# Optimization experiments

Measured on AMD Instinct MI355X. Metric: run time of the kernel, lower is better.

The kernel has to match this reference:

```python
import jax, jax.numpy as jnp
import numpy as np

EMBED_DIM = 2048
HEAD_DIM = 128
B, T = 4, 2048


def setup_inputs() -> dict:
    key = jax.random.key(0)
    k1, k2, k3, k4 = jax.random.split(key, 4)
    x_in = jax.random.normal(k1, (B, T, EMBED_DIM), dtype=jnp.float32)
    scale = 1.0 / np.sqrt(EMBED_DIM)
    Wq = jax.random.normal(k2, (EMBED_DIM, HEAD_DIM), dtype=jnp.float32) * scale
    Wk = jax.random.normal(k3, (EMBED_DIM, HEAD_DIM), dtype=jnp.float32) * scale
    Wv = jax.random.normal(k4, (EMBED_DIM, HEAD_DIM), dtype=jnp.float32) * scale
    return {"x_in": x_in, "Wq": Wq, "Wk": Wk, "Wv": Wv}


def reference(x_in, Wq, Wk, Wv):
    # x_in: [B, T, E]; projections (Linear, no bias)
    q = jnp.einsum('bte,ed->btd', x_in, Wq)  # [B,T,D]
    k = jnp.einsum('bte,ed->btd', x_in, Wk)
    v = jnp.einsum('bte,ed->btd', x_in, Wv)
    t = x_in.shape[1]
    d = Wq.shape[1]
    s = jnp.einsum('btd,bsd->bts', q, k) / jnp.sqrt(jnp.asarray(d, q.dtype))  # [B,Tq,Tk]
    # causal mask: positions with tril==0 (k index > q index) -> -inf
    causal = jnp.tril(jnp.ones((t, t), dtype=bool))
    s = jnp.where(causal, s, -jnp.inf)
    # NOTE: original module applies softmax over dim=1 (query axis), faithfully reproduced
    a = jax.nn.softmax(s, axis=1)
    z = jnp.einsum('bts,bsd->btd', a, v)  # [B,T,D]
    return z
```

## Files before the change

kernel.cpp:

```cpp
#include <hip/hip_runtime.h>

typedef _Float16 f16x8 __attribute__((ext_vector_type(8)));
typedef _Float16 f16x4 __attribute__((ext_vector_type(4)));
typedef float f32x4 __attribute__((ext_vector_type(4)));

#define T_DIM 2048
#define E_DIM 2048
#define D_DIM 128
#define NB 4
#define KSP_P 4
#define KCH_P 512
#define KSP_A 8
#define KCH_A 256
#define NCH2 32

__device__ __forceinline__ void gll16(const void* g, void* l) {
  __builtin_amdgcn_global_load_lds(
      (const __attribute__((address_space(1))) unsigned int*)g,
      (__attribute__((address_space(3))) unsigned int*)l, 16, 0, 0);
}

__device__ __forceinline__ void merge_stat(float& m, float& l, float pm, float pl) {
  if (pm != -__builtin_inff()) {
    float nm = fmaxf(m, pm);
    l = l * __expf(m - nm) + pl * __expf(pm - nm);
    m = nm;
  }
}


__global__ void prep(const float* __restrict__ Wq, const float* __restrict__ Wk,
                     const float* __restrict__ Wv, _Float16* __restrict__ WhT,
                     float* __restrict__ Z) {
  int idx = blockIdx.x * 256 + threadIdx.x;
  int y = blockIdx.y;
  if (y < 3) {
    const float* W = (y == 0) ? Wq : ((y == 1) ? Wk : Wv);
    int e = idx & (E_DIM - 1), d = idx >> 11;
    WhT[(size_t)y * (D_DIM * E_DIM) + idx] = (_Float16)W[e * D_DIM + d];
  } else {
    f32x4 z = {0.f, 0.f, 0.f, 0.f};
    *(f32x4*)(Z + (size_t)idx * 4) = z;
  }
}


__global__ __launch_bounds__(384) void proj_gemm(
    const float* __restrict__ x, const _Float16* __restrict__ WhT,
    _Float16* __restrict__ Ph) {
  __shared__ _Float16 A16[2][64 * 32];
  __shared__ _Float16 Bsw[2][384 * 32];
  const int tid = threadIdx.x, w = tid >> 6, lane = tid & 63;
  const int wn = w, quad = lane >> 4, l16 = lane & 15;
  const int t0 = blockIdx.x * 64;
  const int ks = blockIdx.y;
  const int kb = ks * KCH_P;
  const int arow = tid >> 2, aseg = tid & 3;
  const int asw = (aseg ^ ((arow >> 1) & 3)) * 8;
  const int br = tid >> 2, bseg = tid & 3;

  f32x4 ax0, ax1;
  auto loadA = [&](int k0) {
    if (tid < 256) {
      const float* src = x + (size_t)(t0 + arow) * E_DIM + k0 + aseg * 8;
      ax0 = *(const f32x4*)src;
      ax1 = *(const f32x4*)(src + 4);
    }
  };
  auto writeA = [&](int buf) {
    if (tid < 256) {
      f16x8 o;
#pragma unroll
      for (int e = 0; e < 4; ++e) {
        o[e] = (_Float16)ax0[e];
        o[e + 4] = (_Float16)ax1[e];
      }
      *(f16x8*)(&A16[buf][arow * 32 + asw]) = o;
    }
  };
  auto stageB = [&](int buf, int k0) {
#pragma unroll
    for (int p = 0; p < 4; ++p) {
      int r = p * 96 + br;
      int g = bseg ^ ((r >> 1) & 3);
      gll16(WhT + (size_t)r * E_DIM + k0 + g * 8, &Bsw[buf][r * 32 + bseg * 8]);
    }
  };

  f32x4 acc[4][4] = {};
  loadA(kb);
  stageB(0, kb);
  asm volatile("s_waitcnt vmcnt(0)" ::: "memory");
  writeA(0);
  const int NIT = KCH_P / 32;
  for (int it = 0; it < NIT; ++it) {
    const int cur = it & 1;
    __syncthreads();
    if (it + 1 < NIT) {
      loadA(kb + (it + 1) * 32);
      stageB(cur ^ 1, kb + (it + 1) * 32);
    }
    f16x8 af[4], bf[4];
#pragma unroll
    for (int i = 0; i < 4; ++i) {
      int row = i * 16 + l16;
      int sg = (quad ^ ((row >> 1) & 3)) * 8;
      af[i] = *(const f16x8*)(&A16[cur][row * 32 + sg]);
    }
#pragma unroll
    for (int j = 0; j < 4; ++j) {
      int row = wn * 64 + j * 16 + l16;
      int sg = (quad ^ ((row >> 1) & 3)) * 8;
      bf[j] = *(const f16x8*)(&Bsw[cur][row * 32 + sg]);
    }
    __builtin_amdgcn_s_setprio(1);
#pragma unroll
    for (int i = 0; i < 4; ++i)
#pragma unroll
      for (int j = 0; j < 4; ++j)
        acc[i][j] = __builtin_amdgcn_mfma_f32_16x16x32_f16(af[i], bf[j], acc[i][j], 0, 0, 0);
    __builtin_amdgcn_s_setprio(0);
    if (it + 1 < NIT) {
      asm volatile("s_waitcnt vmcnt(0)" ::: "memory");
      writeA(cur ^ 1);
    }
  }
  const int mat = wn >> 1;
  const int nb0 = (wn & 1) * 64;
  _Float16* P = Ph + ((size_t)(ks * 3 + mat) << 20);
  if (mat < 2) {
#pragma unroll
    for (int i = 0; i < 4; ++i)
#pragma unroll
      for (int j = 0; j < 4; ++j) {
        int n = nb0 + j * 16 + l16;
#pragma unroll
        for (int r = 0; r < 4; ++r) {
          int t = t0 + i * 16 + quad * 4 + r;
          P[(size_t)t * D_DIM + n] = (_Float16)acc[i][j][r];
        }
      }
  } else {
#pragma unroll
    for (int i = 0; i < 4; ++i)
#pragma unroll
      for (int j = 0; j < 4; ++j) {
        int n = nb0 + j * 16 + l16;
        int t = t0 + i * 16 + quad * 4;
        f16x4 o;
#pragma unroll
        for (int r = 0; r < 4; ++r) o[r] = (_Float16)acc[i][j][r];
        *(f16x4*)(P + ((size_t)(t >> 11) * D_DIM + n) * T_DIM + (t & (T_DIM - 1))) = o;
      }
  }
}


__global__ void proj_reduce(const _Float16* __restrict__ Ph, _Float16* __restrict__ Qh,
                            _Float16* __restrict__ Kh, _Float16* __restrict__ VT) {
  size_t u = ((size_t)blockIdx.x * 256 + threadIdx.x) * 8;
  int mat = (int)(u >> 20);
  size_t rem = u & ((1u << 20) - 1);
  float s[8] = {};
#pragma unroll
  for (int ks = 0; ks < KSP_P; ++ks) {
    f16x8 p = *(const f16x8*)(Ph + ((size_t)(ks * 3 + mat) << 20) + rem);
#pragma unroll
    for (int e = 0; e < 8; ++e) s[e] += (float)p[e];
  }
  f16x8 o;
#pragma unroll
  for (int e = 0; e < 8; ++e) o[e] = (_Float16)s[e];
  _Float16* dst = (mat == 0) ? Qh : ((mat == 1) ? Kh : VT);
  *(f16x8*)(dst + rem) = o;
}


__global__ __launch_bounds__(256) void s_gemm(const _Float16* __restrict__ Qh,
                                              const _Float16* __restrict__ Kh,
                                              _Float16* __restrict__ S,
                                              float* __restrict__ Pm,
                                              float* __restrict__ Pl) {
  int idx = blockIdx.x;
  int xt = (int)((sqrtf(8.f * idx + 1.f) - 1.f) * 0.5f);
  while ((xt + 1) * (xt + 2) / 2 <= idx) ++xt;
  while (xt * (xt + 1) / 2 > idx) --xt;
  int yt = idx - xt * (xt + 1) / 2;
  __shared__ _Float16 Bs[4][128 * 32];
  const int tid = threadIdx.x, w = tid >> 6, lane = tid & 63;
  const int wr = w >> 1, wc = w & 1, quad = lane >> 4, l16 = lane & 15;
  const int t0 = xt * 128, s0 = yt * 128, b = blockIdx.y;
  const _Float16* A = Qh + (size_t)b * T_DIM * D_DIM;
  const _Float16* B = Kh + (size_t)b * T_DIM * D_DIM;
  const int srow = lane >> 2;
  const int swz = ((lane & 3) ^ ((srow >> 1) & 3)) * 8;
#pragma unroll
  for (int kq = 0; kq < 4; ++kq)
#pragma unroll
    for (int q = 0; q < 2; ++q) {
      int rbase = w * 32 + q * 16;
      gll16(B + (size_t)(s0 + rbase + srow) * D_DIM + kq * 32 + swz,
            Bs[kq] + rbase * 32);
    }
  __syncthreads();
  f32x4 acc[4][4] = {};
  const int bsg = (quad ^ ((l16 >> 1) & 3)) * 8;
#pragma unroll
  for (int kq = 0; kq < 4; ++kq) {
    f16x8 af[4], bf[4];
#pragma unroll
    for (int i = 0; i < 4; ++i)
      af[i] = *(const f16x8*)(A + (size_t)(t0 + wr * 64 + i * 16 + l16) * D_DIM +
                              kq * 32 + quad * 8);
#pragma unroll
    for (int j = 0; j < 4; ++j)
      bf[j] = *(const f16x8*)(Bs[kq] + (wc * 64 + j * 16 + l16) * 32 + bsg);
#pragma unroll
    for (int i = 0; i < 4; ++i)
#pragma unroll
      for (int j = 0; j < 4; ++j)
        acc[i][j] = __builtin_amdgcn_mfma_f32_16x16x32_f16(af[i], bf[j], acc[i][j], 0, 0, 0);
  }
  _Float16* Sb = S + (size_t)b * T_DIM * T_DIM;
  const float scale = 0.08838834764831845f;
  const float NEG = -__builtin_inff();
#pragma unroll
  for (int j = 0; j < 4; ++j) {
    const int s = s0 + wc * 64 + j * 16 + l16;
    float vv[16];
    float m = NEG;
#pragma unroll
    for (int i = 0; i < 4; ++i)
#pragma unroll
      for (int r = 0; r < 4; ++r) {
        int t = t0 + wr * 64 + i * 16 + quad * 4 + r;
        float v = (s > t) ? NEG : acc[i][j][r] * scale;
        Sb[(size_t)t * T_DIM + s] = (_Float16)v;
        vv[i * 4 + r] = v;
        m = fmaxf(m, v);
      }
    float l = 0.f;
    if (m != NEG) {
#pragma unroll
      for (int k = 0; k < 16; ++k) l += __expf(vv[k] - m);
    }
#pragma unroll
    for (int d = 16; d <= 32; d <<= 1) {
      float pm = __shfl_xor(m, d, 64);
      float pl = __shfl_xor(l, d, 64);
      merge_stat(m, l, pm, pl);
    }
    if (quad == 0) {
      int c = 2 * xt + wr;
      Pm[((size_t)c * NB + b) * T_DIM + s] = m;
      Pl[((size_t)c * NB + b) * T_DIM + s] = l;
    }
  }
}


__global__ __launch_bounds__(256) void av_gemm(const _Float16* __restrict__ S,
                                               const _Float16* __restrict__ VT,
                                               const float* __restrict__ Pm,
                                               const float* __restrict__ Pl,
                                               float* __restrict__ Z) {
  const int t0 = blockIdx.x * 128, b = blockIdx.y, ks = blockIdx.z;
  const int Kmax = t0 + 128;
  const int Kstart = ks * KCH_A;
  if (Kstart >= Kmax) return;
  const int Kend = (Kstart + KCH_A < Kmax) ? (Kstart + KCH_A) : Kmax;
  const int nit = (Kend - Kstart) >> 5;
  __shared__ _Float16 As[2][128 * 32];
  __shared__ _Float16 Bs[2][128 * 32];
  __shared__ float Ms[KCH_A];
  __shared__ float Ls[KCH_A];
  const int tid = threadIdx.x, w = tid >> 6, lane = tid & 63;
  const int wr = w >> 1, wc = w & 1, quad = lane >> 4, l16 = lane & 15;
  const _Float16* Sb = S + (size_t)b * T_DIM * T_DIM;
  const _Float16* Vb = VT + (size_t)b * D_DIM * T_DIM;
  {
    const int s = Kstart + tid;
    const int c0 = s >> 6;
    float m = -__builtin_inff(), l = 0.f;
    for (int base = c0 & ~7; base < NCH2; base += 8) {
      float pm[8], pl[8];
#pragma unroll
      for (int k = 0; k < 8; ++k) {
        size_t pidx = ((size_t)(base + k) * NB + b) * T_DIM + s;
        pm[k] = Pm[pidx];
        pl[k] = Pl[pidx];
      }
#pragma unroll
      for (int k = 0; k < 8; ++k)
        if (base + k >= c0) merge_stat(m, l, pm[k], pl[k]);
    }
    Ms[tid] = m;
    Ls[tid] = 1.f / l;
  }
  __syncthreads();
  const int srow = lane >> 2;
  const int arow = tid >> 2, aseg = tid & 3;
  const int asw = (aseg ^ ((arow >> 1) & 3)) * 8;
  f16x8 sv0, sv1;
  auto loadS = [&](int k0) {
    sv0 = *(const f16x8*)(Sb + (size_t)(t0 + arow) * T_DIM + k0 + aseg * 8);
    sv1 = *(const f16x8*)(Sb + (size_t)(t0 + 64 + arow) * T_DIM + k0 + aseg * 8);
  };
  auto stageB = [&](int buf, int k0) {
#pragma unroll
    for (int q = 0; q < 2; ++q) {
      int rbase = w * 32 + q * 16;
      int row = rbase + srow;
      int g = ((lane & 3) ^ ((row >> 1) & 3)) * 8;
      gll16(Vb + (size_t)row * T_DIM + k0 + g, Bs[buf] + rbase * 32);
    }
  };
  auto writeA = [&](int buf, int k0) {
#pragma unroll
    for (int q = 0; q < 2; ++q) {
      f16x8 v = q ? sv1 : sv0;
      f16x8 o;
#pragma unroll
      for (int e = 0; e < 8; ++e) {
        int li = k0 + aseg * 8 + e - Kstart;
        o[e] = (_Float16)(__expf((float)v[e] - Ms[li]) * Ls[li]);
      }
      *(f16x8*)(As[buf] + (q * 64 + arow) * 32 + asw) = o;
    }
  };
  f32x4 acc[4][4] = {};
  loadS(Kstart);
  stageB(0, Kstart);
  asm volatile("s_waitcnt vmcnt(0)" ::: "memory");
  writeA(0, Kstart);
  for (int it = 0; it < nit; ++it) {
    const int cur = it & 1;
    const int k0 = Kstart + it * 32;
    __syncthreads();
    if (it + 1 < nit) {
      loadS(k0 + 32);
      stageB(cur ^ 1, k0 + 32);
    }
    f16x8 af[4], bf[4];
#pragma unroll
    for (int i = 0; i < 4; ++i) {
      int row = wr * 64 + i * 16 + l16;
      int sg = (quad ^ ((row >> 1) & 3)) * 8;
      af[i] = *(const f16x8*)(As[cur] + row * 32 + sg);
    }
#pragma unroll
    for (int j = 0; j < 4; ++j) {
      int row = wc * 64 + j * 16 + l16;
      int sg = (quad ^ ((row >> 1) & 3)) * 8;
      bf[j] = *(const f16x8*)(Bs[cur] + row * 32 + sg);
    }
    __builtin_amdgcn_s_setprio(1);
#pragma unroll
    for (int i = 0; i < 4; ++i)
#pragma unroll
      for (int j = 0; j < 4; ++j)
        acc[i][j] = __builtin_amdgcn_mfma_f32_16x16x32_f16(af[i], bf[j], acc[i][j], 0, 0, 0);
    __builtin_amdgcn_s_setprio(0);
    if (it + 1 < nit) {
      asm volatile("s_waitcnt vmcnt(0)" ::: "memory");
      writeA(cur ^ 1, k0 + 32);
    }
  }
  float* Zb = Z + (size_t)b * T_DIM * D_DIM;
#pragma unroll
  for (int i = 0; i < 4; ++i)
#pragma unroll
    for (int j = 0; j < 4; ++j) {
      int n = wc * 64 + j * 16 + l16;
#pragma unroll
      for (int r = 0; r < 4; ++r) {
        int t = t0 + wr * 64 + i * 16 + quad * 4 + r;
        atomicAdd(&Zb[(size_t)t * D_DIM + n], acc[i][j][r]);
      }
    }
}


extern "C" void kernel_launch(void* const* d_in, const int* in_sizes, int n_in,
                              void* d_out, int out_size, void* d_ws, size_t ws_size,
                              hipStream_t stream) {
  const float* x = (const float*)d_in[0];
  const float* Wq = (const float*)d_in[1];
  const float* Wk = (const float*)d_in[2];
  const float* Wv = (const float*)d_in[3];
  char* ws = (char*)d_ws;
  _Float16* WhT = (_Float16*)(ws + 33554432);
  _Float16* Qh = (_Float16*)(ws + 35127296);
  _Float16* Kh = (_Float16*)(ws + 37224448);
  _Float16* VT = (_Float16*)(ws + 39321600);
  _Float16* S = (_Float16*)(ws + 41418752);
  _Float16* Ph = (_Float16*)(ws + 41418752);
  float* Pm = (float*)(ws + 75038720);
  float* Pl = (float*)(ws + 76087296);
  float* Z = (float*)d_out;

  prep<<<dim3(1024, 4), 256, 0, stream>>>(Wq, Wk, Wv, WhT, Z);
  proj_gemm<<<dim3(128, KSP_P), 384, 0, stream>>>(x, WhT, Ph);
  proj_reduce<<<1536, 256, 0, stream>>>(Ph, Qh, Kh, VT);
  s_gemm<<<dim3(136, 4), 256, 0, stream>>>(Qh, Kh, S, Pm, Pl);
  av_gemm<<<dim3(16, 4, KSP_A), 256, 0, stream>>>(S, VT, Pm, Pl, Z);
}
```

Baseline: 185.2 us.

## Stage fp32 x via direct-to-LDS loads, single-buffer proj GEMM, double K split

After: 336.8 us. 81.9% more time.

```diff
diff --git a/kernel.cpp b/kernel.cpp
--- a/kernel.cpp
+++ b/kernel.cpp
@@ -8,8 +8,8 @@
 #define E_DIM 2048
 #define D_DIM 128
 #define NB 4
-#define KSP_P 4
-#define KCH_P 512
+#define KSP_P 8
+#define KCH_P 256
 #define KSP_A 8
 #define KCH_A 256
 #define NCH2 32
@@ -45,85 +45,63 @@
 }
 
 
-__global__ __launch_bounds__(384) void proj_gemm(
+__global__ __launch_bounds__(384, 6) void proj_gemm(
     const float* __restrict__ x, const _Float16* __restrict__ WhT,
     _Float16* __restrict__ Ph) {
-  __shared__ _Float16 A16[2][64 * 32];
-  __shared__ _Float16 Bsw[2][384 * 32];
+  __shared__ float Asw[64 * 32];
+  __shared__ _Float16 Bsw[384 * 32];
   const int tid = threadIdx.x, w = tid >> 6, lane = tid & 63;
   const int wn = w, quad = lane >> 4, l16 = lane & 15;
   const int t0 = blockIdx.x * 64;
   const int ks = blockIdx.y;
   const int kb = ks * KCH_P;
-  const int arow = tid >> 2, aseg = tid & 3;
-  const int asw = (aseg ^ ((arow >> 1) & 3)) * 8;
+  const int ar0 = tid >> 3, aseg = tid & 7;
+  const int ar1 = (384 + tid) >> 3;
   const int br = tid >> 2, bseg = tid & 3;
 
-  f32x4 ax0, ax1;
-  auto loadA = [&](int k0) {
-    if (tid < 256) {
-      const float* src = x + (size_t)(t0 + arow) * E_DIM + k0 + aseg * 8;
-      ax0 = *(const f32x4*)src;
-      ax1 = *(const f32x4*)(src + 4);
-    }
-  };
-  auto writeA = [&](int buf) {
-    if (tid < 256) {
-      f16x8 o;
-#pragma unroll
-      for (int e = 0; e < 4; ++e) {
-        o[e] = (_Float16)ax0[e];
-        o[e + 4] = (_Float16)ax1[e];
-      }
-      *(f16x8*)(&A16[buf][arow * 32 + asw]) = o;
-    }
-  };
-  auto stageB = [&](int buf, int k0) {
+  f32x4 acc[4][4] = {};
+  for (int k0 = kb; k0 < kb + KCH_P; k0 += 32) {
+    __syncthreads();
+    {
+      int g = aseg ^ (ar0 & 7);
+      gll16(x + (size_t)(t0 + ar0) * E_DIM + k0 + g * 4, Asw + tid * 4);
+      if (tid < 128) {
+        int g2 = aseg ^ (ar1 & 7);
+        gll16(x + (size_t)(t0 + ar1) * E_DIM + k0 + g2 * 4, Asw + (384 + tid) * 4);
+      }
+    }
 #pragma unroll
     for (int p = 0; p < 4; ++p) {
       int r = p * 96 + br;
       int g = bseg ^ ((r >> 1) & 3);
-      gll16(WhT + (size_t)r * E_DIM + k0 + g * 8, &Bsw[buf][r * 32 + bseg * 8]);
-    }
-  };
-
-  f32x4 acc[4][4] = {};
-  loadA(kb);
-  stageB(0, kb);
-  asm volatile("s_waitcnt vmcnt(0)" ::: "memory");
-  writeA(0);
-  const int NIT = KCH_P / 32;
-  for (int it = 0; it < NIT; ++it) {
-    const int cur = it & 1;
+      gll16(WhT + (size_t)r * E_DIM + k0 + g * 8, Bsw + (p * 384 + tid) * 8);
+    }
     __syncthreads();
-    if (it + 1 < NIT) {
-      loadA(kb + (it + 1) * 32);
-      stageB(cur ^ 1, kb + (it + 1) * 32);
-    }
     f16x8 af[4], bf[4];
 #pragma unroll
     for (int i = 0; i < 4; ++i) {
       int row = i * 16 + l16;
-      int sg = (quad ^ ((row >> 1) & 3)) * 8;
-      af[i] = *(const f16x8*)(&A16[cur][row * 32 + sg]);
+      int s0 = (2 * quad) ^ (row & 7);
+      int s1 = (2 * quad + 1) ^ (row & 7);
+      f32x4 a0 = *(const f32x4*)(Asw + row * 32 + s0 * 4);
+      f32x4 a1 = *(const f32x4*)(Asw + row * 32 + s1 * 4);
+#pragma unroll
+      for (int e = 0; e < 4; ++e) {
+        af[i][e] = (_Float16)a0[e];
+        af[i][e + 4] = (_Float16)a1[e];
+      }
     }
 #pragma unroll
     for (int j = 0; j < 4; ++j) {
       int row = wn * 64 + j * 16 + l16;
       int sg = (quad ^ ((row >> 1) & 3)) * 8;
-      bf[j] = *(const f16x8*)(&Bsw[cur][row * 32 + sg]);
-    }
-    __builtin_amdgcn_s_setprio(1);
+      bf[j] = *(const f16x8*)(Bsw + row * 32 + sg);
+    }
 #pragma unroll
     for (int i = 0; i < 4; ++i)
 #pragma unroll
       for (int j = 0; j < 4; ++j)
         acc[i][j] = __builtin_amdgcn_mfma_f32_16x16x32_f16(af[i], bf[j], acc[i][j], 0, 0, 0);
-    __builtin_amdgcn_s_setprio(0);
-    if (it + 1 < NIT) {
-      asm volatile("s_waitcnt vmcnt(0)" ::: "memory");
-      writeA(cur ^ 1);
-    }
   }
   const int mat = wn >> 1;
   const int nb0 = (wn & 1) * 64;
@@ -389,14 +367,14 @@
   const float* Wk = (const float*)d_in[2];
   const float* Wv = (const float*)d_in[3];
   char* ws = (char*)d_ws;
-  _Float16* WhT = (_Float16*)(ws + 33554432);
-  _Float16* Qh = (_Float16*)(ws + 35127296);
-  _Float16* Kh = (_Float16*)(ws + 37224448);
-  _Float16* VT = (_Float16*)(ws + 39321600);
-  _Float16* S = (_Float16*)(ws + 41418752);
-  _Float16* Ph = (_Float16*)(ws + 41418752);
-  float* Pm = (float*)(ws + 75038720);
-  float* Pl = (float*)(ws + 76087296);
+  _Float16* Ph = (_Float16*)(ws);
+  _Float16* S = (_Float16*)(ws);
+  _Float16* WhT = (_Float16*)(ws + 50331648);
+  _Float16* Qh = (_Float16*)(ws + 51904512);
+  _Float16* Kh = (_Float16*)(ws + 54001664);
+  _Float16* VT = (_Float16*)(ws + 56098816);
+  float* Pm = (float*)(ws + 58195968);
+  float* Pl = (float*)(ws + 59244544);
   float* Z = (float*)d_out;
 
   prep<<<dim3(1024, 4), 256, 0, stream>>>(Wq, Wk, Wv, WhT, Z);
```

## Drop max-subtraction in softmax, store exp scores and atomically sum column denominators

Applied to the files above, without the earlier changes.

New measurement: 173.1 us. 1.07x faster.

```diff
diff --git a/kernel.cpp b/kernel.cpp
--- a/kernel.cpp
+++ b/kernel.cpp
@@ -8,11 +8,10 @@
 #define E_DIM 2048
 #define D_DIM 128
 #define NB 4
-#define KSP_P 4
-#define KCH_P 512
+#define KSP_P 8
+#define KCH_P 256
 #define KSP_A 8
 #define KCH_A 256
-#define NCH2 32
 
 __device__ __forceinline__ void gll16(const void* g, void* l) {
   __builtin_amdgcn_global_load_lds(
@@ -20,18 +19,10 @@
       (__attribute__((address_space(3))) unsigned int*)l, 16, 0, 0);
 }
 
-__device__ __forceinline__ void merge_stat(float& m, float& l, float pm, float pl) {
-  if (pm != -__builtin_inff()) {
-    float nm = fmaxf(m, pm);
-    l = l * __expf(m - nm) + pl * __expf(pm - nm);
-    m = nm;
-  }
-}
-
 
 __global__ void prep(const float* __restrict__ Wq, const float* __restrict__ Wk,
                      const float* __restrict__ Wv, _Float16* __restrict__ WhT,
-                     float* __restrict__ Z) {
+                     float* __restrict__ Z, float* __restrict__ L) {
   int idx = blockIdx.x * 256 + threadIdx.x;
   int y = blockIdx.y;
   if (y < 3) {
@@ -41,50 +32,50 @@
   } else {
     f32x4 z = {0.f, 0.f, 0.f, 0.f};
     *(f32x4*)(Z + (size_t)idx * 4) = z;
-  }
-}
-
-
-__global__ __launch_bounds__(384) void proj_gemm(
+    if (idx < NB * T_DIM) L[idx] = 0.f;
+  }
+}
+
+
+__global__ __launch_bounds__(768) void proj_gemm(
     const float* __restrict__ x, const _Float16* __restrict__ WhT,
     _Float16* __restrict__ Ph) {
-  __shared__ _Float16 A16[2][64 * 32];
+  __shared__ _Float16 A16[2][128 * 32];
   __shared__ _Float16 Bsw[2][384 * 32];
   const int tid = threadIdx.x, w = tid >> 6, lane = tid & 63;
-  const int wn = w, quad = lane >> 4, l16 = lane & 15;
-  const int t0 = blockIdx.x * 64;
+  const int wn = w >> 1, wr = w & 1, quad = lane >> 4, l16 = lane & 15;
+  const int t0 = blockIdx.x * 128;
   const int ks = blockIdx.y;
   const int kb = ks * KCH_P;
-  const int arow = tid >> 2, aseg = tid & 3;
-  const int asw = (aseg ^ ((arow >> 1) & 3)) * 8;
+  const int arowA = tid >> 2, asegA = tid & 3;
+  const int aswA = (asegA ^ ((arowA >> 1) & 3)) * 8;
   const int br = tid >> 2, bseg = tid & 3;
 
   f32x4 ax0, ax1;
   auto loadA = [&](int k0) {
-    if (tid < 256) {
-      const float* src = x + (size_t)(t0 + arow) * E_DIM + k0 + aseg * 8;
+    if (tid < 512) {
+      const float* src = x + (size_t)(t0 + arowA) * E_DIM + k0 + asegA * 8;
       ax0 = *(const f32x4*)src;
       ax1 = *(const f32x4*)(src + 4);
     }
   };
   auto writeA = [&](int buf) {
-    if (tid < 256) {
+    if (tid < 512) {
       f16x8 o;
 #pragma unroll
       for (int e = 0; e < 4; ++e) {
         o[e] = (_Float16)ax0[e];
         o[e + 4] = (_Float16)ax1[e];
       }
-      *(f16x8*)(&A16[buf][arow * 32 + asw]) = o;
+      *(f16x8*)(&A16[buf][arowA * 32 + aswA]) = o;
     }
   };
   auto stageB = [&](int buf, int k0) {
-#pragma unroll
-    for (int p = 0; p < 4; ++p) {
-      int r = p * 96 + br;
-      int g = bseg ^ ((r >> 1) & 3);
-      gll16(WhT + (size_t)r * E_DIM + k0 + g * 8, &Bsw[buf][r * 32 + bseg * 8]);
-    }
+    int g = bseg ^ ((br >> 1) & 3);
+    gll16(WhT + (size_t)br * E_DIM + k0 + g * 8, &Bsw[buf][br * 32 + bseg * 8]);
+    int r = 192 + br;
+    int g2 = bseg ^ ((r >> 1) & 3);
+    gll16(WhT + (size_t)r * E_DIM + k0 + g2 * 8, &Bsw[buf][r * 32 + bseg * 8]);
   };
 
   f32x4 acc[4][4] = {};
@@ -103,7 +94,7 @@
     f16x8 af[4], bf[4];
 #pragma unroll
     for (int i = 0; i < 4; ++i) {
-      int row = i * 16 + l16;
+      int row = wr * 64 + i * 16 + l16;
       int sg = (quad ^ ((row >> 1) & 3)) * 8;
       af[i] = *(const f16x8*)(&A16[cur][row * 32 + sg]);
     }
@@ -136,7 +127,7 @@
         int n = nb0 + j * 16 + l16;
 #pragma unroll
         for (int r = 0; r < 4; ++r) {
-          int t = t0 + i * 16 + quad * 4 + r;
+          int t = t0 + wr * 64 + i * 16 + quad * 4 + r;
           P[(size_t)t * D_DIM + n] = (_Float16)acc[i][j][r];
         }
       }
@@ -146,7 +137,7 @@
 #pragma unroll
       for (int j = 0; j < 4; ++j) {
         int n = nb0 + j * 16 + l16;
-        int t = t0 + i * 16 + quad * 4;
+        int t = t0 + wr * 64 + i * 16 + quad * 4;
         f16x4 o;
 #pragma unroll
         for (int r = 0; r < 4; ++r) o[r] = (_Float16)acc[i][j][r];
@@ -179,8 +170,7 @@
 __global__ __launch_bounds__(256) void s_gemm(const _Float16* __restrict__ Qh,
                                               const _Float16* __restrict__ Kh,
                                               _Float16* __restrict__ S,
-                                              float* __restrict__ Pm,
-                                              float* __restrict__ Pl) {
+                                              float* __restrict__ L) {
   int idx = blockIdx.x;
   int xt = (int)((sqrtf(8.f * idx + 1.f) - 1.f) * 0.5f);
   while ((xt + 1) * (xt + 2) / 2 <= idx) ++xt;
@@ -223,46 +213,29 @@
   }
   _Float16* Sb = S + (size_t)b * T_DIM * T_DIM;
   const float scale = 0.08838834764831845f;
-  const float NEG = -__builtin_inff();
 #pragma unroll
   for (int j = 0; j < 4; ++j) {
     const int s = s0 + wc * 64 + j * 16 + l16;
-    float vv[16];
-    float m = NEG;
+    float l = 0.f;
 #pragma unroll
     for (int i = 0; i < 4; ++i)
 #pragma unroll
       for (int r = 0; r < 4; ++r) {
         int t = t0 + wr * 64 + i * 16 + quad * 4 + r;
-        float v = (s > t) ? NEG : acc[i][j][r] * scale;
-        Sb[(size_t)t * T_DIM + s] = (_Float16)v;
-        vv[i * 4 + r] = v;
-        m = fmaxf(m, v);
-      }
-    float l = 0.f;
-    if (m != NEG) {
-#pragma unroll
-      for (int k = 0; k < 16; ++k) l += __expf(vv[k] - m);
-    }
-#pragma unroll
-    for (int d = 16; d <= 32; d <<= 1) {
-      float pm = __shfl_xor(m, d, 64);
-      float pl = __shfl_xor(l, d, 64);
-      merge_stat(m, l, pm, pl);
-    }
-    if (quad == 0) {
-      int c = 2 * xt + wr;
-      Pm[((size_t)c * NB + b) * T_DIM + s] = m;
-      Pl[((size_t)c * NB + b) * T_DIM + s] = l;
-    }
+        float e = (s > t) ? 0.f : __expf(acc[i][j][r] * scale);
+        Sb[(size_t)t * T_DIM + s] = (_Float16)e;
+        l += e;
+      }
+    l += __shfl_xor(l, 16, 64);
+    l += __shfl_xor(l, 32, 64);
+    if (quad == 0) atomicAdd(&L[(size_t)b * T_DIM + s], l);
   }
 }
 
 
 __global__ __launch_bounds__(256) void av_gemm(const _Float16* __restrict__ S,
                                                const _Float16* __restrict__ VT,
-                                               const float* __restrict__ Pm,
-                                               const float* __restrict__ Pl,
+                                               const float* __restrict__ L,
                                                float* __restrict__ Z) {
   const int t0 = blockIdx.x * 128, b = blockIdx.y, ks = blockIdx.z;
   const int Kmax = t0 + 128;
@@ -272,32 +245,13 @@
   const int nit = (Kend - Kstart) >> 5;
   __shared__ _Float16 As[2][128 * 32];
   __shared__ _Float16 Bs[2][128 * 32];
-  __shared__ float Ms[KCH_A];
   __shared__ float Ls[KCH_A];
   const int tid = threadIdx.x, w = tid >> 6, lane = tid & 63;
   const int wr = w >> 1, wc = w & 1, quad = lane >> 4, l16 = lane & 15;
   const _Float16* Sb = S + (size_t)b * T_DIM * T_DIM;
   const _Float16* Vb = VT + (size_t)b * D_DIM * T_DIM;
-  {
-    const int s = Kstart + tid;
-    const int c0 = s >> 6;
-    float m = -__builtin_inff(), l = 0.f;
-    for (int base = c0 & ~7; base < NCH2; base += 8) {
-      float pm[8], pl[8];
-#pragma unroll
-      for (int k = 0; k < 8; ++k) {
-        size_t pidx = ((size_t)(base + k) * NB + b) * T_DIM + s;
-        pm[k] = Pm[pidx];
-        pl[k] = Pl[pidx];
-      }
-#pragma unroll
-      for (int k = 0; k < 8; ++k)
-        if (base + k >= c0) merge_stat(m, l, pm[k], pl[k]);
-    }
-    Ms[tid] = m;
-    Ls[tid] = 1.f / l;
-  }
-  __syncthreads();
+  for (int i = tid; i < Kend - Kstart; i += 256)
+    Ls[i] = 1.f / L[b * T_DIM + Kstart + i];
   const int srow = lane >> 2;
   const int arow = tid >> 2, aseg = tid & 3;
   const int asw = (aseg ^ ((arow >> 1) & 3)) * 8;
@@ -323,12 +277,13 @@
 #pragma unroll
       for (int e = 0; e < 8; ++e) {
         int li = k0 + aseg * 8 + e - Kstart;
-        o[e] = (_Float16)(__expf((float)v[e] - Ms[li]) * Ls[li]);
+        o[e] = (_Float16)((float)v[e] * Ls[li]);
       }
       *(f16x8*)(As[buf] + (q * 64 + arow) * 32 + asw) = o;
     }
   };
   f32x4 acc[4][4] = {};
+  __syncthreads();
   loadS(Kstart);
   stageB(0, Kstart);
   asm volatile("s_waitcnt vmcnt(0)" ::: "memory");
@@ -389,19 +344,18 @@
   const float* Wk = (const float*)d_in[2];
   const float* Wv = (const float*)d_in[3];
   char* ws = (char*)d_ws;
-  _Float16* WhT = (_Float16*)(ws + 33554432);
-  _Float16* Qh = (_Float16*)(ws + 35127296);
-  _Float16* Kh = (_Float16*)(ws + 37224448);
-  _Float16* VT = (_Float16*)(ws + 39321600);
-  _Float16* S = (_Float16*)(ws + 41418752);
-  _Float16* Ph = (_Float16*)(ws + 41418752);
-  float* Pm = (float*)(ws + 75038720);
-  float* Pl = (float*)(ws + 76087296);
+  _Float16* Ph = (_Float16*)(ws);
+  _Float16* S = (_Float16*)(ws);
+  _Float16* WhT = (_Float16*)(ws + 50331648);
+  _Float16* Qh = (_Float16*)(ws + 51904512);
+  _Float16* Kh = (_Float16*)(ws + 54001664);
+  _Float16* VT = (_Float16*)(ws + 56098816);
+  float* L = (float*)(ws + 58195968);
   float* Z = (float*)d_out;
 
-  prep<<<dim3(1024, 4), 256, 0, stream>>>(Wq, Wk, Wv, WhT, Z);
-  proj_gemm<<<dim3(128, KSP_P), 384, 0, stream>>>(x, WhT, Ph);
+  prep<<<dim3(1024, 4), 256, 0, stream>>>(Wq, Wk, Wv, WhT, Z, L);
+  proj_gemm<<<dim3(64, KSP_P), 768, 0, stream>>>(x, WhT, Ph);
   proj_reduce<<<1536, 256, 0, stream>>>(Ph, Qh, Kh, VT);
-  s_gemm<<<dim3(136, 4), 256, 0, stream>>>(Qh, Kh, S, Pm, Pl);
-  av_gemm<<<dim3(16, 4, KSP_A), 256, 0, stream>>>(S, VT, Pm, Pl, Z);
-}
+  s_gemm<<<dim3(136, 4), 256, 0, stream>>>(Qh, Kh, S, L);
+  av_gemm<<<dim3(16, 4, KSP_A), 256, 0, stream>>>(S, VT, L, Z);
+}
```
